# Kernel optimization log

Measured on AMD Instinct MI355X. Metric: run time of the kernel, lower is better.

The kernel has to match this reference:

```python
import jax, jax.numpy as jnp
import numpy as np

N = 50000      # nodes
E = 400000     # edges (before self-loops)
NFEAT = 256
NHID = 64
NHEAD = 8
NOUT = 128


def gat_conv(h, src, dst, W, attn_l, attn_r, bias, n, H, D):
    """DGL GATConv (eval mode: feat_drop/attn_drop are no-ops), negative_slope=0.2."""
    feat = (h @ W).reshape(n, H, D)                      # [N,H,D]
    el = jnp.einsum('nhd,hd->nh', feat, attn_l)          # [N,H]
    er = jnp.einsum('nhd,hd->nh', feat, attn_r)          # [N,H]
    e = jax.nn.leaky_relu(el[src] + er[dst], 0.2)        # [E,H]
    # segment softmax over incoming edges of each dst node
    m = jax.ops.segment_max(e, dst, num_segments=n)      # [N,H] (every node has a self-loop)
    ex = jnp.exp(e - m[dst])
    denom = jax.ops.segment_sum(ex, dst, num_segments=n)
    a = ex / denom[dst]                                  # [E,H]
    rst = jax.ops.segment_sum(a[:, :, None] * feat[src], dst, num_segments=n)  # [N,H,D]
    return rst + bias.reshape(1, H, D)


def setup_inputs() -> dict:
    key = jax.random.key(0)
    ks = jax.random.split(key, 10)
    s = 0.1
    x = jax.random.normal(ks[0], (N, NFEAT), jnp.float32)
    edge_index = jax.random.randint(ks[1], (2, E), 0, N, dtype=jnp.int64)
    W1 = jax.random.normal(ks[2], (NFEAT, NHEAD * NHID), jnp.float32) * s
    al1 = jax.random.normal(ks[3], (NHEAD, NHID), jnp.float32) * s
    ar1 = jax.random.normal(ks[4], (NHEAD, NHID), jnp.float32) * s
    b1 = jax.random.normal(ks[5], (NHEAD * NHID,), jnp.float32) * s
    W2 = jax.random.normal(ks[6], (NHEAD * NHID, NOUT), jnp.float32) * s
    al2 = jax.random.normal(ks[7], (1, NOUT), jnp.float32) * s
    ar2 = jax.random.normal(ks[8], (1, NOUT), jnp.float32) * s
    b2 = jax.random.normal(ks[9], (NOUT,), jnp.float32) * s
    return {"x": x, "edge_index": edge_index, "W1": W1, "al1": al1, "ar1": ar1,
            "b1": b1, "W2": W2, "al2": al2, "ar2": ar2, "b2": b2}


def reference(x, edge_index, W1, al1, ar1, b1, W2, al2, ar2, b2):
    n = x.shape[0]
    loop = jnp.arange(n, dtype=edge_index.dtype)
    src = jnp.concatenate([edge_index[0], loop])  # dgl.add_self_loop
    dst = jnp.concatenate([edge_index[1], loop])
    # hidden layer (dropout is identity in eval mode)
    h = gat_conv(x, src, dst, W1, al1, ar1, b1, n, NHEAD, NHID).reshape(n, NFEAT * 2)
    h = jax.nn.elu(h)
    out = gat_conv(h, src, dst, W2, al2, ar2, b2, n, 1, NOUT).reshape(n, NOUT)
    return out
```

## Files before the change

### kernel.cpp

```cpp
#include <hip/hip_runtime.h>

#define NFEAT 256
#define NHID 64
#define NHEAD 8
#define HID1 512
#define NOUT 128

typedef unsigned short ushort_t;
typedef unsigned int uint_t;
typedef __attribute__((ext_vector_type(8))) short short8;
typedef __attribute__((ext_vector_type(4))) float floatx4;
typedef __attribute__((ext_vector_type(4))) ushort_t ushort4_t;

static __device__ __forceinline__ float bf2f(uint_t s) {
    return __uint_as_float(s << 16);
}
static __device__ __forceinline__ ushort_t f2bf(float f) {
    uint_t u = __float_as_uint(f);
    u += 0x7FFF + ((u >> 16) & 1);
    return (ushort_t)(u >> 16);
}

__global__ void k_prep(const float* __restrict__ x, ushort_t* __restrict__ xb,
                       const float* __restrict__ W1, ushort_t* __restrict__ W1t,
                       const float* __restrict__ W2, ushort_t* __restrict__ W2t,
                       const int* __restrict__ dstA, int* __restrict__ deg,
                       int n, int E, int c0, int c1, int c2) {
    int blk = blockIdx.x;
    int t = threadIdx.x;
    if (blk < c0) {
        int i = blk * 256 + t;
        floatx4 f = ((const floatx4*)x)[i];
        ushort4_t o;
        #pragma unroll
        for (int j = 0; j < 4; ++j) o[j] = f2bf(f[j]);
        ((ushort4_t*)xb)[i] = o;
    } else if (blk < c1) {
        int i = (blk - c0) * 256 + t;
        int nn = i / NFEAT, kk = i % NFEAT;
        W1t[i] = f2bf(W1[(size_t)kk * HID1 + nn]);
    } else if (blk < c2) {
        int i = (blk - c1) * 256 + t;
        int nn = i / HID1, kk = i % HID1;
        W2t[i] = f2bf(W2[(size_t)kk * NOUT + nn]);
    } else {
        int i = (blk - c2) * 256 + t;
        if (i < E + n) {
            int d = (i < E) ? dstA[i] : (i - E);
            atomicAdd(&deg[d], 1);
        }
    }
}

__global__ __launch_bounds__(1024) void k_scan(const int* __restrict__ deg, int* __restrict__ indptr, int n) {
    __shared__ int part[1024];
    int t = threadIdx.x;
    int chunk = (n + 1023) >> 10;
    int b = t * chunk;
    int e = min(b + chunk, n);
    int s = 0;
    int i = b;
    for (; i + 3 < e; i += 4)
        s += (deg[i] + deg[i + 1]) + (deg[i + 2] + deg[i + 3]);
    for (; i < e; ++i) s += deg[i];
    part[t] = s;
    __syncthreads();
    for (int off = 1; off < 1024; off <<= 1) {
        int v = (t >= off) ? part[t - off] : 0;
        __syncthreads();
        part[t] += v;
        __syncthreads();
    }
    int run = (t == 0) ? 0 : part[t - 1];
    i = b;
    for (; i + 3 < e; i += 4) {
        int d0 = deg[i], d1 = deg[i + 1], d2 = deg[i + 2], d3 = deg[i + 3];
        indptr[i] = run; run += d0;
        indptr[i + 1] = run; run += d1;
        indptr[i + 2] = run; run += d2;
        indptr[i + 3] = run; run += d3;
    }
    for (; i < e; ++i) { indptr[i] = run; run += deg[i]; }
    if (t == 1023) indptr[n] = part[1023];
}

__global__ void k_fillw(const int* __restrict__ srcA, const int* __restrict__ dstA, int E, int n,
                        const int* __restrict__ indptr, int* __restrict__ cnt,
                        int* __restrict__ csr_src,
                        const float* __restrict__ el, const float* __restrict__ er,
                        float* __restrict__ wcsr) {
    int i = blockIdx.x * blockDim.x + threadIdx.x;
    if (i >= E + n) return;
    int s, d;
    if (i < E) { s = srcA[i]; d = dstA[i]; } else { s = i - E; d = s; }
    int pos = indptr[d] + atomicAdd(&cnt[d], 1);
    csr_src[pos] = s;
    floatx4 el0 = *(const floatx4*)(el + (size_t)s * NHEAD);
    floatx4 el1v = *(const floatx4*)(el + (size_t)s * NHEAD + 4);
    floatx4 er0 = *(const floatx4*)(er + (size_t)d * NHEAD);
    floatx4 er1v = *(const floatx4*)(er + (size_t)d * NHEAD + 4);
    floatx4 w0, w1;
    #pragma unroll
    for (int h = 0; h < 4; ++h) {
        float xa = el0[h] + er0[h];
        xa = (xa > 0.f) ? xa : 0.2f * xa;
        w0[h] = __expf(xa);
        float xb2 = el1v[h] + er1v[h];
        xb2 = (xb2 > 0.f) ? xb2 : 0.2f * xb2;
        w1[h] = __expf(xb2);
    }
    *(floatx4*)(wcsr + (size_t)pos * NHEAD) = w0;
    *(floatx4*)(wcsr + (size_t)pos * NHEAD + 4) = w1;
}

__global__ __launch_bounds__(256) void k_gemm1(const ushort_t* __restrict__ A,
                                               const ushort_t* __restrict__ Bt,
                                               ushort_t* __restrict__ C,
                                               const float* __restrict__ al,
                                               const float* __restrict__ ar,
                                               float* __restrict__ el, float* __restrict__ er,
                                               int M) {
    const int N = HID1, K = NFEAT;
    __shared__ __align__(16) ushort_t As[128 * 32];
    __shared__ __align__(16) ushort_t Bs[256 * 32];
    const int t = threadIdx.x;
    const int w = t >> 6, lane = t & 63;
    const int l16 = lane & 15, quad = lane >> 4;
    const int m0 = blockIdx.y * 128, n0 = blockIdx.x * 256;
    const int r0 = (w >> 1) * 64;
    const int c0 = (w & 1) * 128;

    floatx4 acc[4][8] = {};

    const int skp = (t & 3) * 8;
    for (int k0 = 0; k0 < K; k0 += 32) {
        #pragma unroll
        for (int j = 0; j < 2; ++j) {
            int r = (j * 256 + t) >> 2;
            int gr = m0 + r; if (gr >= M) gr = M - 1;
            const ushort_t* gp = A + (size_t)gr * K + k0 + skp;
            __builtin_amdgcn_global_load_lds((const __attribute__((address_space(1))) void*)gp,
                (__attribute__((address_space(3))) void*)(As + (j * 256 + (t & ~63)) * 8), 16, 0, 0);
        }
        #pragma unroll
        for (int j = 0; j < 4; ++j) {
            int r = (j * 256 + t) >> 2;
            const ushort_t* gp = Bt + (size_t)(n0 + r) * K + k0 + skp;
            __builtin_amdgcn_global_load_lds((const __attribute__((address_space(1))) void*)gp,
                (__attribute__((address_space(3))) void*)(Bs + (j * 256 + (t & ~63)) * 8), 16, 0, 0);
        }
        __syncthreads();

        short8 af[4], bf[8];
        #pragma unroll
        for (int i = 0; i < 4; ++i)
            af[i] = *(const short8*)(As + (r0 + i * 16 + l16) * 32 + quad * 8);
        #pragma unroll
        for (int j = 0; j < 8; ++j)
            bf[j] = *(const short8*)(Bs + (c0 + j * 16 + l16) * 32 + quad * 8);
        #pragma unroll
        for (int i = 0; i < 4; ++i)
            #pragma unroll
            for (int j = 0; j < 8; ++j)
                acc[i][j] = __builtin_amdgcn_mfma_f32_16x16x32_bf16(af[i], bf[j], acc[i][j], 0, 0, 0);
        __syncthreads();
    }

    #pragma unroll
    for (int i = 0; i < 4; ++i) {
        #pragma unroll
        for (int r = 0; r < 4; ++r) {
            int row = m0 + r0 + i * 16 + quad * 4 + r;
            if (row < M) {
                #pragma unroll
                for (int j = 0; j < 8; ++j)
                    C[(size_t)row * N + n0 + c0 + j * 16 + l16] = f2bf(acc[i][j][r]);
            }
        }
    }

    float alv[8], arv[8];
    #pragma unroll
    for (int j = 0; j < 8; ++j) {
        int col = n0 + c0 + j * 16 + l16;
        alv[j] = al[col];
        arv[j] = ar[col];
    }
    int head0 = (n0 + c0) >> 6;
    #pragma unroll
    for (int i = 0; i < 4; ++i) {
        #pragma unroll
        for (int r = 0; r < 4; ++r) {
            float pa = acc[i][0][r] * alv[0] + acc[i][1][r] * alv[1]
                     + acc[i][2][r] * alv[2] + acc[i][3][r] * alv[3];
            float qa = acc[i][0][r] * arv[0] + acc[i][1][r] * arv[1]
                     + acc[i][2][r] * arv[2] + acc[i][3][r] * arv[3];
            float pb = acc[i][4][r] * alv[4] + acc[i][5][r] * alv[5]
                     + acc[i][6][r] * alv[6] + acc[i][7][r] * alv[7];
            float qb = acc[i][4][r] * arv[4] + acc[i][5][r] * arv[5]
                     + acc[i][6][r] * arv[6] + acc[i][7][r] * arv[7];
            #pragma unroll
            for (int o = 8; o > 0; o >>= 1) {
                pa += __shfl_down(pa, o);
                qa += __shfl_down(qa, o);
                pb += __shfl_down(pb, o);
                qb += __shfl_down(qb, o);
            }
            if (l16 == 0) {
                int row = m0 + r0 + i * 16 + quad * 4 + r;
                if (row < M) {
                    el[row * NHEAD + head0] = pa;
                    er[row * NHEAD + head0] = qa;
                    el[row * NHEAD + head0 + 1] = pb;
                    er[row * NHEAD + head0 + 1] = qb;
                }
            }
        }
    }
}

__global__ __launch_bounds__(256) void k_gemm2(const ushort_t* __restrict__ A,
                                               const ushort_t* __restrict__ Bt,
                                               ushort_t* __restrict__ C,
                                               const float* __restrict__ al,
                                               const float* __restrict__ ar,
                                               float* __restrict__ el, float* __restrict__ er,
                                               int M) {
    const int N = NOUT, K = HID1;
    __shared__ __align__(16) ushort_t As[64 * 32];
    __shared__ __align__(16) ushort_t Bs[128 * 32];
    __shared__ float elp[64][2], erp[64][2];
    const int t = threadIdx.x;
    const int w = t >> 6, lane = t & 63;
    const int l16 = lane & 15, quad = lane >> 4;
    const int m0 = blockIdx.y * 64;
    const int r0 = (w >> 1) * 32;
    const int c0 = (w & 1) * 64;

    floatx4 acc[2][4] = {};

    const int arow = t >> 2;
    const int skp = (t & 3) * 8;
    const int wbaseA = (t & ~63) * 8;

    for (int k0 = 0; k0 < K; k0 += 32) {
        int gr = m0 + arow; if (gr >= M) gr = M - 1;
        const ushort_t* gpa = A + (size_t)gr * K + k0 + skp;
        __builtin_amdgcn_global_load_lds((const __attribute__((address_space(1))) void*)gpa,
            (__attribute__((address_space(3))) void*)(As + wbaseA), 16, 0, 0);
        #pragma unroll
        for (int j = 0; j < 2; ++j) {
            int r = (j * 256 + t) >> 2;
            const ushort_t* gpb = Bt + (size_t)r * K + k0 + skp;
            __builtin_amdgcn_global_load_lds((const __attribute__((address_space(1))) void*)gpb,
                (__attribute__((address_space(3))) void*)(Bs + (j * 256 + (t & ~63)) * 8), 16, 0, 0);
        }
        __syncthreads();

        short8 af[2], bf[4];
        #pragma unroll
        for (int i = 0; i < 2; ++i)
            af[i] = *(const short8*)(As + (r0 + i * 16 + l16) * 32 + quad * 8);
        #pragma unroll
        for (int j = 0; j < 4; ++j)
            bf[j] = *(const short8*)(Bs + (c0 + j * 16 + l16) * 32 + quad * 8);
        #pragma unroll
        for (int i = 0; i < 2; ++i)
            #pragma unroll
            for (int j = 0; j < 4; ++j)
                acc[i][j] = __builtin_amdgcn_mfma_f32_16x16x32_bf16(af[i], bf[j], acc[i][j], 0, 0, 0);
        __syncthreads();
    }

    float alv[4], arv[4];
    #pragma unroll
    for (int j = 0; j < 4; ++j) {
        int col = c0 + j * 16 + l16;
        alv[j] = al[col];
        arv[j] = ar[col];
    }
    #pragma unroll
    for (int i = 0; i < 2; ++i) {
        #pragma unroll
        for (int r = 0; r < 4; ++r) {
            int lrow = r0 + i * 16 + quad * 4 + r;
            int row = m0 + lrow;
            if (row < M) {
                #pragma unroll
                for (int j = 0; j < 4; ++j)
                    C[(size_t)row * N + c0 + j * 16 + l16] = f2bf(acc[i][j][r]);
            }
            float p = acc[i][0][r] * alv[0] + acc[i][1][r] * alv[1]
                    + acc[i][2][r] * alv[2] + acc[i][3][r] * alv[3];
            float q = acc[i][0][r] * arv[0] + acc[i][1][r] * arv[1]
                    + acc[i][2][r] * arv[2] + acc[i][3][r] * arv[3];
            #pragma unroll
            for (int o = 8; o > 0; o >>= 1) {
                p += __shfl_down(p, o);
                q += __shfl_down(q, o);
            }
            if (l16 == 0) {
                elp[lrow][w & 1] = p;
                erp[lrow][w & 1] = q;
            }
        }
    }
    __syncthreads();
    if (t < 64) {
        int row = m0 + t;
        if (row < M) {
            el[row] = elp[t][0] + elp[t][1];
            er[row] = erp[t][0] + erp[t][1];
        }
    }
}

__global__ __launch_bounds__(256) void k_agg1(const uint_t* __restrict__ fb, const float* __restrict__ wcsr,
                                              const float* __restrict__ b1,
                                              const int* __restrict__ indptr, const int* __restrict__ csr_src,
                                              uint_t* __restrict__ h1b, int n) {
    int node = blockIdx.x;
    int t = threadIdx.x;
    int h = t >> 5;
    int e0 = indptr[node], e1 = indptr[node + 1];
    float a0 = 0.f, a1 = 0.f, den = 0.f;
    int e = e0;
    for (; e + 3 < e1; e += 4) {
        int s0 = csr_src[e], s1 = csr_src[e + 1], s2 = csr_src[e + 2], s3 = csr_src[e + 3];
        float w0 = wcsr[(size_t)e * NHEAD + h];
        float w1 = wcsr[(size_t)(e + 1) * NHEAD + h];
        float w2 = wcsr[(size_t)(e + 2) * NHEAD + h];
        float w3 = wcsr[(size_t)(e + 3) * NHEAD + h];
        uint_t u0 = fb[(size_t)s0 * 256 + t];
        uint_t u1 = fb[(size_t)s1 * 256 + t];
        uint_t u2 = fb[(size_t)s2 * 256 + t];
        uint_t u3 = fb[(size_t)s3 * 256 + t];
        den += (w0 + w1) + (w2 + w3);
        a0 += w0 * bf2f(u0 & 0xFFFF) + w1 * bf2f(u1 & 0xFFFF)
            + w2 * bf2f(u2 & 0xFFFF) + w3 * bf2f(u3 & 0xFFFF);
        a1 += w0 * bf2f(u0 >> 16) + w1 * bf2f(u1 >> 16)
            + w2 * bf2f(u2 >> 16) + w3 * bf2f(u3 >> 16);
    }
    for (; e < e1; ++e) {
        int s = csr_src[e];
        float w = wcsr[(size_t)e * NHEAD + h];
        uint_t u = fb[(size_t)s * 256 + t];
        den += w;
        a0 += w * bf2f(u & 0xFFFF);
        a1 += w * bf2f(u >> 16);
    }
    float inv = 1.f / den;
    float v0 = a0 * inv + b1[2 * t];
    float v1 = a1 * inv + b1[2 * t + 1];
    v0 = (v0 > 0.f) ? v0 : (__expf(v0) - 1.f);
    v1 = (v1 > 0.f) ? v1 : (__expf(v1) - 1.f);
    h1b[(size_t)node * 256 + t] = (uint_t)f2bf(v0) | ((uint_t)f2bf(v1) << 16);
}

__global__ __launch_bounds__(256) void k_agg2(const uint_t* __restrict__ fb2,
                                              const float* __restrict__ el2, const float* __restrict__ er2,
                                              const float* __restrict__ b2,
                                              const int* __restrict__ indptr, const int* __restrict__ csr_src,
                                              float* __restrict__ out, int n) {
    __shared__ float wch[4][64];
    __shared__ int sch[4][64];
    int w = threadIdx.x >> 6;
    int wid = blockIdx.x * 4 + w;
    int lane = threadIdx.x & 63;
    if (wid >= n) return;
    float erv = er2[wid];
    int e0 = indptr[wid], e1 = indptr[wid + 1];
    int deg = e1 - e0;
    float a0 = 0.f, a1 = 0.f, den = 0.f;

    for (int base = 0; base < deg; base += 64) {
        int cnt = min(64, deg - base);
        if (lane < cnt) {
            int s = csr_src[e0 + base + lane];
            sch[w][lane] = s;
            float x = el2[s] + erv;
            x = (x > 0.f) ? x : 0.2f * x;
            wch[w][lane] = __expf(x);
        }
        __builtin_amdgcn_wave_barrier();
        int e = 0;
        for (; e + 3 < cnt; e += 4) {
            int s0 = sch[w][e], s1 = sch[w][e + 1], s2 = sch[w][e + 2], s3 = sch[w][e + 3];
            float w0 = wch[w][e], w1 = wch[w][e + 1], w2 = wch[w][e + 2], w3 = wch[w][e + 3];
            uint_t u0 = fb2[(size_t)s0 * 64 + lane];
            uint_t u1 = fb2[(size_t)s1 * 64 + lane];
            uint_t u2 = fb2[(size_t)s2 * 64 + lane];
            uint_t u3 = fb2[(size_t)s3 * 64 + lane];
            den += (w0 + w1) + (w2 + w3);
            a0 += w0 * bf2f(u0 & 0xFFFF) + w1 * bf2f(u1 & 0xFFFF)
                + w2 * bf2f(u2 & 0xFFFF) + w3 * bf2f(u3 & 0xFFFF);
            a1 += w0 * bf2f(u0 >> 16) + w1 * bf2f(u1 >> 16)
                + w2 * bf2f(u2 >> 16) + w3 * bf2f(u3 >> 16);
        }
        for (; e < cnt; ++e) {
            int s = sch[w][e];
            float ww = wch[w][e];
            uint_t u = fb2[(size_t)s * 64 + lane];
            den += ww;
            a0 += ww * bf2f(u & 0xFFFF);
            a1 += ww * bf2f(u >> 16);
        }
        __builtin_amdgcn_wave_barrier();
    }

    float inv = 1.f / den;
    float2 o;
    o.x = a0 * inv + b2[2 * lane];
    o.y = a1 * inv + b2[2 * lane + 1];
    ((float2*)out)[(size_t)wid * 64 + lane] = o;
}

extern "C" void kernel_launch(void* const* d_in, const int* in_sizes, int n_in,
                              void* d_out, int out_size, void* d_ws, size_t ws_size,
                              hipStream_t stream) {
    const float* x   = (const float*)d_in[0];
    const int*   ei  = (const int*)d_in[1];
    const float* W1  = (const float*)d_in[2];
    const float* al1 = (const float*)d_in[3];
    const float* ar1 = (const float*)d_in[4];
    const float* b1  = (const float*)d_in[5];
    const float* W2  = (const float*)d_in[6];
    const float* al2 = (const float*)d_in[7];
    const float* ar2 = (const float*)d_in[8];
    const float* b2  = (const float*)d_in[9];

    const int n  = in_sizes[0] / NFEAT;
    const int E  = in_sizes[1] / 2;
    const int ET = E + n;
    const int* srcA = ei;
    const int* dstA = ei + E;

    char* ws = (char*)d_ws;
    size_t off = 0;
    auto alloc = [&](size_t bytes) -> void* {
        void* p = ws + off;
        off += (bytes + 255) & ~(size_t)255;
        return p;
    };
    ushort_t* xb     = (ushort_t*)alloc((size_t)n * NFEAT * 2);
    ushort_t* feat1b = (ushort_t*)alloc((size_t)n * HID1 * 2);
    ushort_t* h1b    = (ushort_t*)alloc((size_t)n * HID1 * 2);
    ushort_t* feat2b = (ushort_t*)alloc((size_t)n * NOUT * 2);
    ushort_t* W1t    = (ushort_t*)alloc((size_t)NFEAT * HID1 * 2);
    ushort_t* W2t    = (ushort_t*)alloc((size_t)HID1 * NOUT * 2);
    float* el1 = (float*)alloc((size_t)n * NHEAD * 4);
    float* er1 = (float*)alloc((size_t)n * NHEAD * 4);
    float* el2 = (float*)alloc((size_t)n * 4);
    float* er2 = (float*)alloc((size_t)n * 4);
    float* wcsr1 = (float*)alloc((size_t)ET * NHEAD * 4);
    int* indptr = (int*)alloc((size_t)(n + 1) * 4);
    int* deg    = (int*)alloc((size_t)2 * n * 4);
    int* cnt    = deg + n;
    int* csr    = (int*)alloc((size_t)ET * 4);

    hipMemsetAsync(deg, 0, (size_t)2 * n * 4, stream);

    const int c0 = (n * NFEAT / 4) / 256;
    const int c1 = c0 + (NFEAT * HID1) / 256;
    const int c2 = c1 + (HID1 * NOUT) / 256;
    const int c3 = c2 + (ET + 255) / 256;
    k_prep<<<c3, 256, 0, stream>>>(x, xb, W1, W1t, W2, W2t, dstA, deg, n, E, c0, c1, c2);

    k_scan<<<1, 1024, 0, stream>>>(deg, indptr, n);

    k_gemm1<<<dim3(HID1 / 256, (n + 127) / 128), 256, 0, stream>>>(xb, W1t, feat1b, al1, ar1, el1, er1, n);
    k_fillw<<<(ET + 255) / 256, 256, 0, stream>>>(srcA, dstA, E, n, indptr, cnt, csr, el1, er1, wcsr1);
    k_agg1<<<n, 256, 0, stream>>>((const uint_t*)feat1b, wcsr1, b1, indptr, csr, (uint_t*)h1b, n);

    k_gemm2<<<dim3(1, (n + 63) / 64), 256, 0, stream>>>(h1b, W2t, feat2b, al2, ar2, el2, er2, n);
    k_agg2<<<(n + 3) / 4, 256, 0, stream>>>((const uint_t*)feat2b, el2, er2, b2, indptr, csr, (float*)d_out, n);
}
```

Measured before the change: 384.2 us.

## Widen GEMM K/M tiles and use a scan-initialized cursor for CSR fill

k_scan now writes a cursor array seeded with the row offsets, so k_fillw gets the CSR slot from a single atomicAdd without also reading indptr, and the memset shrinks. k_gemm1 stages a 64-wide K slice per iteration (two 32-wide chunks), which halves the number of barrier-separated load/compute rounds. k_gemm2 grows its row tile from 64 to 128 per block, doubling the accumulators per wave and halving the block count so each B tile is reused across more rows. Both GEMM changes raise LDS use or register pressure, which could lower occupancy.

```diff
diff --git a/kernel.cpp b/kernel.cpp
--- a/kernel.cpp
+++ b/kernel.cpp
@@ -52,7 +52,8 @@
     }
 }
 
-__global__ __launch_bounds__(1024) void k_scan(const int* __restrict__ deg, int* __restrict__ indptr, int n) {
+__global__ __launch_bounds__(1024) void k_scan(const int* __restrict__ deg, int* __restrict__ indptr,
+                                               int* __restrict__ cursor, int n) {
     __shared__ int part[1024];
     int t = threadIdx.x;
     int chunk = (n + 1023) >> 10;
@@ -75,25 +76,24 @@
     i = b;
     for (; i + 3 < e; i += 4) {
         int d0 = deg[i], d1 = deg[i + 1], d2 = deg[i + 2], d3 = deg[i + 3];
-        indptr[i] = run; run += d0;
-        indptr[i + 1] = run; run += d1;
-        indptr[i + 2] = run; run += d2;
-        indptr[i + 3] = run; run += d3;
-    }
-    for (; i < e; ++i) { indptr[i] = run; run += deg[i]; }
+        indptr[i] = run; cursor[i] = run; run += d0;
+        indptr[i + 1] = run; cursor[i + 1] = run; run += d1;
+        indptr[i + 2] = run; cursor[i + 2] = run; run += d2;
+        indptr[i + 3] = run; cursor[i + 3] = run; run += d3;
+    }
+    for (; i < e; ++i) { indptr[i] = run; cursor[i] = run; run += deg[i]; }
     if (t == 1023) indptr[n] = part[1023];
 }
 
 __global__ void k_fillw(const int* __restrict__ srcA, const int* __restrict__ dstA, int E, int n,
-                        const int* __restrict__ indptr, int* __restrict__ cnt,
-                        int* __restrict__ csr_src,
+                        int* __restrict__ cursor, int* __restrict__ csr_src,
                         const float* __restrict__ el, const float* __restrict__ er,
                         float* __restrict__ wcsr) {
     int i = blockIdx.x * blockDim.x + threadIdx.x;
     if (i >= E + n) return;
     int s, d;
     if (i < E) { s = srcA[i]; d = dstA[i]; } else { s = i - E; d = s; }
-    int pos = indptr[d] + atomicAdd(&cnt[d], 1);
+    int pos = atomicAdd(&cursor[d], 1);
     csr_src[pos] = s;
     floatx4 el0 = *(const floatx4*)(el + (size_t)s * NHEAD);
     floatx4 el1v = *(const floatx4*)(el + (size_t)s * NHEAD + 4);
@@ -121,8 +121,8 @@
                                                float* __restrict__ el, float* __restrict__ er,
                                                int M) {
     const int N = HID1, K = NFEAT;
-    __shared__ __align__(16) ushort_t As[128 * 32];
-    __shared__ __align__(16) ushort_t Bs[256 * 32];
+    __shared__ __align__(16) ushort_t As[2 * 128 * 32];
+    __shared__ __align__(16) ushort_t Bs[2 * 256 * 32];
     const int t = threadIdx.x;
     const int w = t >> 6, lane = t & 63;
     const int l16 = lane & 15, quad = lane >> 4;
@@ -132,37 +132,41 @@
 
     floatx4 acc[4][8] = {};
 
-    const int skp = (t & 3) * 8;
-    for (int k0 = 0; k0 < K; k0 += 32) {
-        #pragma unroll
-        for (int j = 0; j < 2; ++j) {
-            int r = (j * 256 + t) >> 2;
-            int gr = m0 + r; if (gr >= M) gr = M - 1;
-            const ushort_t* gp = A + (size_t)gr * K + k0 + skp;
+    for (int k0 = 0; k0 < K; k0 += 64) {
+        #pragma unroll
+        for (int j = 0; j < 4; ++j) {
+            int gr = m0 + (j & 1) * 64 + (t >> 2);
+            if (gr >= M) gr = M - 1;
+            int koff = k0 + (j >> 1) * 32 + (t & 3) * 8;
+            const ushort_t* gp = A + (size_t)gr * K + koff;
             __builtin_amdgcn_global_load_lds((const __attribute__((address_space(1))) void*)gp,
-                (__attribute__((address_space(3))) void*)(As + (j * 256 + (t & ~63)) * 8), 16, 0, 0);
-        }
-        #pragma unroll
-        for (int j = 0; j < 4; ++j) {
-            int r = (j * 256 + t) >> 2;
-            const ushort_t* gp = Bt + (size_t)(n0 + r) * K + k0 + skp;
+                (__attribute__((address_space(3))) void*)(As + j * 2048 + (t & ~63) * 8), 16, 0, 0);
+        }
+        #pragma unroll
+        for (int j = 0; j < 8; ++j) {
+            int br = n0 + (j & 3) * 64 + (t >> 2);
+            int koff = k0 + (j >> 2) * 32 + (t & 3) * 8;
+            const ushort_t* gp = Bt + (size_t)br * K + koff;
             __builtin_amdgcn_global_load_lds((const __attribute__((address_space(1))) void*)gp,
-                (__attribute__((address_space(3))) void*)(Bs + (j * 256 + (t & ~63)) * 8), 16, 0, 0);
-        }
-        __syncthreads();
-
-        short8 af[4], bf[8];
-        #pragma unroll
-        for (int i = 0; i < 4; ++i)
-            af[i] = *(const short8*)(As + (r0 + i * 16 + l16) * 32 + quad * 8);
-        #pragma unroll
-        for (int j = 0; j < 8; ++j)
-            bf[j] = *(const short8*)(Bs + (c0 + j * 16 + l16) * 32 + quad * 8);
-        #pragma unroll
-        for (int i = 0; i < 4; ++i)
+                (__attribute__((address_space(3))) void*)(Bs + j * 2048 + (t & ~63) * 8), 16, 0, 0);
+        }
+        __syncthreads();
+
+        #pragma unroll
+        for (int c = 0; c < 2; ++c) {
+            short8 af[4], bf[8];
+            #pragma unroll
+            for (int i = 0; i < 4; ++i)
+                af[i] = *(const short8*)(As + c * 4096 + (r0 + i * 16 + l16) * 32 + quad * 8);
             #pragma unroll
             for (int j = 0; j < 8; ++j)
-                acc[i][j] = __builtin_amdgcn_mfma_f32_16x16x32_bf16(af[i], bf[j], acc[i][j], 0, 0, 0);
+                bf[j] = *(const short8*)(Bs + c * 8192 + (c0 + j * 16 + l16) * 32 + quad * 8);
+            #pragma unroll
+            for (int i = 0; i < 4; ++i)
+                #pragma unroll
+                for (int j = 0; j < 8; ++j)
+                    acc[i][j] = __builtin_amdgcn_mfma_f32_16x16x32_bf16(af[i], bf[j], acc[i][j], 0, 0, 0);
+        }
         __syncthreads();
     }
 
@@ -227,45 +231,42 @@
                                                float* __restrict__ el, float* __restrict__ er,
                                                int M) {
     const int N = NOUT, K = HID1;
-    __shared__ __align__(16) ushort_t As[64 * 32];
+    __shared__ __align__(16) ushort_t As[128 * 32];
     __shared__ __align__(16) ushort_t Bs[128 * 32];
-    __shared__ float elp[64][2], erp[64][2];
+    __shared__ float elp[128][2], erp[128][2];
     const int t = threadIdx.x;
     const int w = t >> 6, lane = t & 63;
     const int l16 = lane & 15, quad = lane >> 4;
-    const int m0 = blockIdx.y * 64;
-    const int r0 = (w >> 1) * 32;
+    const int m0 = blockIdx.y * 128;
+    const int r0 = (w >> 1) * 64;
     const int c0 = (w & 1) * 64;
 
-    floatx4 acc[2][4] = {};
-
-    const int arow = t >> 2;
+    floatx4 acc[4][4] = {};
+
     const int skp = (t & 3) * 8;
-    const int wbaseA = (t & ~63) * 8;
-
     for (int k0 = 0; k0 < K; k0 += 32) {
-        int gr = m0 + arow; if (gr >= M) gr = M - 1;
-        const ushort_t* gpa = A + (size_t)gr * K + k0 + skp;
-        __builtin_amdgcn_global_load_lds((const __attribute__((address_space(1))) void*)gpa,
-            (__attribute__((address_space(3))) void*)(As + wbaseA), 16, 0, 0);
         #pragma unroll
         for (int j = 0; j < 2; ++j) {
             int r = (j * 256 + t) >> 2;
+            int gr = m0 + r; if (gr >= M) gr = M - 1;
+            const ushort_t* gpa = A + (size_t)gr * K + k0 + skp;
+            __builtin_amdgcn_global_load_lds((const __attribute__((address_space(1))) void*)gpa,
+                (__attribute__((address_space(3))) void*)(As + (j * 256 + (t & ~63)) * 8), 16, 0, 0);
             const ushort_t* gpb = Bt + (size_t)r * K + k0 + skp;
             __builtin_amdgcn_global_load_lds((const __attribute__((address_space(1))) void*)gpb,
                 (__attribute__((address_space(3))) void*)(Bs + (j * 256 + (t & ~63)) * 8), 16, 0, 0);
         }
         __syncthreads();
 
-        short8 af[2], bf[4];
-        #pragma unroll
-        for (int i = 0; i < 2; ++i)
+        short8 af[4], bf[4];
+        #pragma unroll
+        for (int i = 0; i < 4; ++i)
             af[i] = *(const short8*)(As + (r0 + i * 16 + l16) * 32 + quad * 8);
         #pragma unroll
         for (int j = 0; j < 4; ++j)
             bf[j] = *(const short8*)(Bs + (c0 + j * 16 + l16) * 32 + quad * 8);
         #pragma unroll
-        for (int i = 0; i < 2; ++i)
+        for (int i = 0; i < 4; ++i)
             #pragma unroll
             for (int j = 0; j < 4; ++j)
                 acc[i][j] = __builtin_amdgcn_mfma_f32_16x16x32_bf16(af[i], bf[j], acc[i][j], 0, 0, 0);
@@ -280,7 +281,7 @@
         arv[j] = ar[col];
     }
     #pragma unroll
-    for (int i = 0; i < 2; ++i) {
+    for (int i = 0; i < 4; ++i) {
         #pragma unroll
         for (int r = 0; r < 4; ++r) {
             int lrow = r0 + i * 16 + quad * 4 + r;
@@ -306,7 +307,7 @@
         }
     }
     __syncthreads();
-    if (t < 64) {
+    if (t < 128) {
         int row = m0 + t;
         if (row < M) {
             el[row] = elp[t][0] + elp[t][1];
@@ -454,11 +455,11 @@
     float* er2 = (float*)alloc((size_t)n * 4);
     float* wcsr1 = (float*)alloc((size_t)ET * NHEAD * 4);
     int* indptr = (int*)alloc((size_t)(n + 1) * 4);
-    int* deg    = (int*)alloc((size_t)2 * n * 4);
-    int* cnt    = deg + n;
+    int* cursor = (int*)alloc((size_t)n * 4);
+    int* deg    = (int*)alloc((size_t)n * 4);
     int* csr    = (int*)alloc((size_t)ET * 4);
 
-    hipMemsetAsync(deg, 0, (size_t)2 * n * 4, stream);
+    hipMemsetAsync(deg, 0, (size_t)n * 4, stream);
 
     const int c0 = (n * NFEAT / 4) / 256;
     const int c1 = c0 + (NFEAT * HID1) / 256;
@@ -466,12 +467,12 @@
     const int c3 = c2 + (ET + 255) / 256;
     k_prep<<<c3, 256, 0, stream>>>(x, xb, W1, W1t, W2, W2t, dstA, deg, n, E, c0, c1, c2);
 
-    k_scan<<<1, 1024, 0, stream>>>(deg, indptr, n);
+    k_scan<<<1, 1024, 0, stream>>>(deg, indptr, cursor, n);
 
     k_gemm1<<<dim3(HID1 / 256, (n + 127) / 128), 256, 0, stream>>>(xb, W1t, feat1b, al1, ar1, el1, er1, n);
-    k_fillw<<<(ET + 255) / 256, 256, 0, stream>>>(srcA, dstA, E, n, indptr, cnt, csr, el1, er1, wcsr1);
+    k_fillw<<<(ET + 255) / 256, 256, 0, stream>>>(srcA, dstA, E, n, cursor, csr, el1, er1, wcsr1);
     k_agg1<<<n, 256, 0, stream>>>((const uint_t*)feat1b, wcsr1, b1, indptr, csr, (uint_t*)h1b, n);
 
-    k_gemm2<<<dim3(1, (n + 63) / 64), 256, 0, stream>>>(h1b, W2t, feat2b, al2, ar2, el2, er2, n);
+    k_gemm2<<<dim3(1, (n + 127) / 128), 256, 0, stream>>>(h1b, W2t, feat2b, al2, ar2, el2, er2, n);
     k_agg2<<<(n + 3) / 4, 256, 0, stream>>>((const uint_t*)feat2b, el2, er2, b2, indptr, csr, (float*)d_out, n);
 }
```

Measured after the change: 393.6 us. 1.02x slower.
